# Kernel optimization log

Hardware: AMD Instinct MI355X
Metric: run time of the kernel (lower is better)

## Reference

```python
import jax, jax.numpy as jnp
import numpy as np

H = 16        # num attention heads
KVH = 4       # num key/value heads
D = 128       # head dim
WIN = 1024    # sliding window (in packed per-state positions)
THETA = 10000.0
NUM_STATES = 8


def rotate_half(x):
    half = x.shape[-1] // 2
    return jnp.concatenate([-x[..., half:], x[..., :half]], axis=-1)


def setup_inputs() -> dict:
    key = jax.random.key(0)
    ks = jax.random.split(key, 6)
    B, L, HID = 2, 2048, 2048
    s = 0.02
    hidden_states = jax.random.normal(ks[0], (B, L, HID), jnp.float32)
    Wq = jax.random.normal(ks[1], (H * D, HID), jnp.float32) * s
    Wk = jax.random.normal(ks[2], (KVH * D, HID), jnp.float32) * s
    Wv = jax.random.normal(ks[3], (KVH * D, HID), jnp.float32) * s
    Wo = jax.random.normal(ks[4], (HID, H * D), jnp.float32) * s
    sid = jax.random.randint(ks[5], (B, L), 0, NUM_STATES).astype(jnp.int64)
    position_ids = jnp.tile(jnp.arange(L, dtype=jnp.int64)[None, :], (B, 1))
    return dict(hidden_states=hidden_states, Wq=Wq, Wk=Wk, Wv=Wv, Wo=Wo,
                sid=sid, position_ids=position_ids)


def reference(hidden_states, Wq, Wk, Wv, Wo, sid, position_ids):
    B, L, HID = hidden_states.shape
    # projections (Linear without bias: x @ W.T)
    q = (hidden_states @ Wq.T).reshape(B, L, H, D)
    k = (hidden_states @ Wk.T).reshape(B, L, KVH, D)
    v = (hidden_states @ Wv.T).reshape(B, L, KVH, D)
    # rotary embedding
    inv_freq = 1.0 / (THETA ** (jnp.arange(0, D, 2, dtype=jnp.float32) / D))
    freqs = position_ids.astype(jnp.float32)[:, :, None] * inv_freq[None, None, :]  # [B,L,D/2]
    emb = jnp.concatenate([freqs, freqs], axis=-1)                                  # [B,L,D]
    cos = jnp.cos(emb)[:, :, None, :].astype(hidden_states.dtype)
    sin = jnp.sin(emb)[:, :, None, :].astype(hidden_states.dtype)
    q = q * cos + rotate_half(q) * sin
    k = k * cos + rotate_half(k) * sin
    # GQA: repeat kv heads (repeat_interleave along head dim)
    n_rep = H // KVH
    k = jnp.repeat(k, n_rep, axis=2)  # [B,L,H,D]
    v = jnp.repeat(v, n_rep, axis=2)
    # BoSs mask: attend within same state id, causal, sliding window over
    # packed-per-state rank distance (equivalent to the varlen packing path)
    same = sid[:, :, None] == sid[:, None, :]                  # [B,L,L]
    tril = jnp.tril(jnp.ones((L, L), dtype=bool))[None]        # [1,L,L]
    rank = jnp.sum(same & tril, axis=-1) - 1                   # [B,L] rank within own state
    win_ok = (rank[:, :, None] - rank[:, None, :]) <= WIN
    mask = same & tril & win_ok                                # [B,L,L]
    scale = D ** -0.5
    scores = jnp.einsum('bqhd,bkhd->bhqk', q, k) * scale       # [B,H,L,L]
    scores = jnp.where(mask[:, None, :, :], scores, jnp.finfo(scores.dtype).min)
    attn = jax.nn.softmax(scores, axis=-1)
    o = jnp.einsum('bhqk,bkhd->bqhd', attn, v).reshape(B, L, H * D)
    return o @ Wo.T
```

## Files before the change

### kernel.cpp

```cpp
#include <hip/hip_runtime.h>
#include <hip/hip_bf16.h>

#define H_ 16
#define KVH_ 4
#define D_ 128
#define L_ 2048
#define B_ 2
#define HID_ 2048
#define WIN_ 1024
#define NS_ 8
#define QKV_N 3072

typedef __attribute__((ext_vector_type(8))) short short8;
typedef __attribute__((ext_vector_type(4))) float floatx4;

__device__ inline float bf16_to_f(unsigned short u) {
    union { unsigned int i; float f; } c; c.i = ((unsigned int)u) << 16; return c.f;
}
__device__ inline unsigned short f_to_bf16(float f) {
    __hip_bfloat16 h = __float2bfloat16(f);
    return *(unsigned short*)&h;
}

__device__ inline int world_is_bf16(const unsigned short* hs_u) {
    int lane = threadIdx.x & 63;
    unsigned short u = hs_u[(lane & 31) * 2];
    int e = (u >> 7) & 0xFF;
    unsigned long long bad = __ballot(e > 130);
    return bad == 0ULL;
}
__device__ inline int pid_stride(const int* pids) { return (pids[1] == 0) ? 2 : 1; }

__global__ __launch_bounds__(256) void convert_all(const void* __restrict__ hs,
                                                   const void* __restrict__ Wq,
                                                   const void* __restrict__ Wk,
                                                   const void* __restrict__ Wv,
                                                   const void* __restrict__ Wo,
                                                   unsigned short* __restrict__ c_hs,
                                                   unsigned short* __restrict__ c_Wq,
                                                   unsigned short* __restrict__ c_Wk,
                                                   unsigned short* __restrict__ c_Wv,
                                                   unsigned short* __restrict__ c_Wo) {
    int isbf = world_is_bf16((const unsigned short*)hs);
    if (isbf) return;
    const int N0 = (B_ * L_ * HID_) / 4;
    const int N1 = (HID_ * HID_) / 4;
    const int N2 = (KVH_ * D_ * HID_) / 4;
    const int N3 = N2;
    const int N4 = N1;
    const int total = N0 + N1 + N2 + N3 + N4;
    for (int i = blockIdx.x * 256 + threadIdx.x; i < total; i += gridDim.x * 256) {
        int j = i;
        const void* src; unsigned short* dst;
        if (j < N0)              { src = hs; dst = c_hs; }
        else if ((j -= N0) < N1) { src = Wq; dst = c_Wq; }
        else if ((j -= N1) < N2) { src = Wk; dst = c_Wk; }
        else if ((j -= N2) < N3) { src = Wv; dst = c_Wv; }
        else                     { j -= N3; src = Wo; dst = c_Wo; }
        float4 f = ((const float4*)src)[j];
        ushort4 o4;
        o4.x = f_to_bf16(f.x); o4.y = f_to_bf16(f.y);
        o4.z = f_to_bf16(f.z); o4.w = f_to_bf16(f.w);
        ((ushort4*)dst)[j] = o4;
    }
}

__global__ __launch_bounds__(256) void scan_kernel(const int* __restrict__ sid,
                                                   const int* __restrict__ pids,
                                                   int* __restrict__ rank,
                                                   int* __restrict__ poslist,
                                                   int* __restrict__ counts) {
    int stride = pid_stride(pids);
    int b = blockIdx.x;
    int t = threadIdx.x;
    __shared__ int cnt[256][NS_];
    __shared__ int pre[256][NS_];
    const int* s = sid + (size_t)b * L_ * stride;
    int myid[8];
#pragma unroll
    for (int i = 0; i < 8; i++) myid[i] = s[(t * 8 + i) * stride];
#pragma unroll
    for (int st = 0; st < NS_; st++) cnt[t][st] = 0;
#pragma unroll
    for (int i = 0; i < 8; i++) cnt[t][myid[i]]++;
    __syncthreads();
    for (int off = 1; off < 256; off <<= 1) {
        int add[NS_];
        if (t >= off)
#pragma unroll
            for (int st = 0; st < NS_; st++) add[st] = cnt[t - off][st];
        __syncthreads();
        if (t >= off)
#pragma unroll
            for (int st = 0; st < NS_; st++) cnt[t][st] += add[st];
        __syncthreads();
    }
#pragma unroll
    for (int st = 0; st < NS_; st++) pre[t][st] = t ? cnt[t - 1][st] : 0;
    if (t == 255)
#pragma unroll
        for (int st = 0; st < NS_; st++) counts[b * NS_ + st] = cnt[255][st];
    __syncthreads();
#pragma unroll
    for (int i = 0; i < 8; i++) {
        int sd = myid[i];
        int r = pre[t][sd]++;
        int pos = t * 8 + i;
        rank[b * L_ + pos] = r;
        poslist[((size_t)b * NS_ + sd) * L_ + r] = pos;
    }
}

#define STAGE(gptr, ldsdst)                                                     \
    __builtin_amdgcn_global_load_lds(                                           \
        (const __attribute__((address_space(1))) unsigned int*)(gptr),          \
        (__attribute__((address_space(3))) unsigned int*)(ldsdst), 16, 0, 0)

#define SB __builtin_amdgcn_sched_barrier(0)

#define MFMA_P(P)                                                               \
    __builtin_amdgcn_s_setprio(1);                                              \
    _Pragma("unroll")                                                           \
    for (int m2 = 0; m2 < 2; ++m2)                                              \
        _Pragma("unroll")                                                       \
        for (int nt = 0; nt < 4; ++nt)                                          \
            acc[(P) * 2 + m2][nt] = __builtin_amdgcn_mfma_f32_16x16x32_bf16(    \
                fA[(P) * 2 + m2], fB[nt], acc[(P) * 2 + m2][nt], 0, 0, 0);      \
    __builtin_amdgcn_s_setprio(0)

template<int MT>
__global__ __launch_bounds__(512, 1) void gemm_t(const unsigned short* __restrict__ Ac,
                                                 const unsigned short* __restrict__ B0c,
                                                 const unsigned short* __restrict__ B1c,
                                                 const unsigned short* __restrict__ B2c,
                                                 const unsigned short* __restrict__ Aa,
                                                 const unsigned short* __restrict__ B0a,
                                                 const unsigned short* __restrict__ B1a,
                                                 const unsigned short* __restrict__ B2a,
                                                 void* __restrict__ C,
                                                 int M, int N, int K,
                                                 int nb1, int nb2,
                                                 const unsigned short* __restrict__ hs_probe,
                                                 int c_mode) {
    const int CH_A = MT / 2;
    __shared__ unsigned short As[4][MT * 2048];
    __shared__ unsigned short Bs[4][8192];
    int tid = threadIdx.x;
    int wave = tid >> 6, lane = tid & 63;
    int quad = lane >> 4, l16 = lane & 15;
    int wr = wave >> 2, wc = wave & 3;
    int bn_t = blockIdx.x;
    int bm = blockIdx.y * (MT * 64), bn = bn_t * 256;

    int isbf = world_is_bf16(hs_probe);
    const unsigned short* A  = isbf ? Aa  : Ac;
    const unsigned short* B0 = isbf ? B0a : B0c;
    const unsigned short* B1 = isbf ? B1a : B1c;
    const unsigned short* B2 = isbf ? B2a : B2c;

    const unsigned short* Bseg;
    int brow0;
    if (bn_t < nb1)      { Bseg = B0; brow0 = bn; }
    else if (bn_t < nb2) { Bseg = B1; brow0 = bn - nb1 * 256; }
    else                 { Bseg = B2; brow0 = bn - nb2 * 256; }

    int sub = tid >> 2, slot = tid & 3;
    int swz = slot ^ ((sub >> 1) & 3);
    unsigned int a_off[CH_A], b_off[2];
#pragma unroll
    for (int c = 0; c < CH_A; ++c)
        a_off[c] = (unsigned int)((bm + c * 128 + sub) * K + swz * 8);
#pragma unroll
    for (int c = 0; c < 2; ++c)
        b_off[c] = (unsigned int)((brow0 + c * 128 + sub) * K + swz * 8);

    const int arow = wr * (MT * 32) + l16;
    const int brr  = wc * 64 + l16;
    const int xr   = (l16 >> 1) & 3;

    floatx4 acc[2 * MT][4] = {};
    short8 fA[2 * MT], fB[4];
    const int KT = K >> 5;

#pragma unroll
    for (int pt = 0; pt < 3; ++pt) {
        unsigned int kel = (unsigned int)pt * 32;
#pragma unroll
        for (int c = 0; c < 2; ++c)
            STAGE(Bseg + b_off[c] + kel, &Bs[pt][c * 4096 + tid * 8]);
#pragma unroll
        for (int c = 0; c < CH_A; ++c)
            STAGE(A + a_off[c] + kel, &As[pt][c * 4096 + tid * 8]);
    }

    for (int t = 0; t < KT; ++t) {
        const unsigned short* Ab = As[t & 3];
        const unsigned short* Bb = Bs[t & 3];
        int nbuf = (t + 3) & 3;
        int t3 = (t + 3 < KT) ? t + 3 : KT - 1;
        unsigned int kel = (unsigned int)t3 * 32;

        if constexpr (MT == 4) asm volatile("s_waitcnt vmcnt(8)" ::: "memory");
        else                   asm volatile("s_waitcnt vmcnt(6)" ::: "memory");
        __builtin_amdgcn_s_barrier();
        asm volatile("" ::: "memory");

#pragma unroll
        for (int nt = 0; nt < 4; ++nt)
            fB[nt] = *(const short8*)&Bb[(brr + nt * 16) * 32 + ((quad ^ xr) * 8)];
#pragma unroll
        for (int mt = 0; mt < 2 * MT; ++mt)
            fA[mt] = *(const short8*)&Ab[(arow + mt * 16) * 32 + ((quad ^ xr) * 8)];
        SB;

#pragma unroll
        for (int c = 0; c < 2; ++c)
            STAGE(Bseg + b_off[c] + kel, &Bs[nbuf][c * 4096 + tid * 8]);
#pragma unroll
        for (int c = 0; c < CH_A; ++c)
            STAGE(A + a_off[c] + kel, &As[nbuf][c * 4096 + tid * 8]);
        SB;

        MFMA_P(0); SB;
        MFMA_P(1);
        if constexpr (MT == 4) {
            SB; MFMA_P(2); SB; MFMA_P(3);
        }
    }
    asm volatile("s_waitcnt vmcnt(0)" ::: "memory");

    int cf32 = c_mode ? !isbf : 0;
#pragma unroll
    for (int a = 0; a < 2 * MT; ++a)
#pragma unroll
        for (int g = 0; g < 4; ++g)
#pragma unroll
            for (int r = 0; r < 4; ++r) {
                int row = bm + wr * (MT * 32) + a * 16 + quad * 4 + r;
                int col = bn + wc * 64 + g * 16 + l16;
                size_t idx = (size_t)row * N + col;
                if (cf32) ((float*)C)[idx] = acc[a][g][r];
                else      ((unsigned short*)C)[idx] = f_to_bf16(acc[a][g][r]);
            }
}

__global__ __launch_bounds__(256) void rope_kernel(unsigned short* __restrict__ qkv,
                                                   const int* __restrict__ pos_ids) {
    int stride = pid_stride(pos_ids);
    int idx = blockIdx.x * 256 + threadIdx.x;
    int i = idx & 31;
    int tmp = idx >> 5;
    int head = tmp % 20;
    int bl = tmp / 20;
    if (bl >= B_ * L_) return;
    float posf = (float)pos_ids[bl * stride];
    const float k = (2.0f / 128.0f) * 13.287712379549449f;
    float inv0 = exp2f(-(float)(2 * i) * k);
    float inv1 = exp2f(-(float)(2 * i + 1) * k);
    float a0 = posf * inv0, a1 = posf * inv1;
    float c0 = cosf(a0), s0 = sinf(a0);
    float c1 = cosf(a1), s1 = sinf(a1);
    unsigned short* p = qkv + (size_t)bl * QKV_N +
                        ((head < H_) ? head * D_ : 2048 + (head - H_) * D_);
    ushort2 lo = *(const ushort2*)(p + 2 * i);
    ushort2 hi = *(const ushort2*)(p + 2 * i + 64);
    float x0a = bf16_to_f(lo.x), x0b = bf16_to_f(lo.y);
    float x1a = bf16_to_f(hi.x), x1b = bf16_to_f(hi.y);
    ushort2 olo, ohi;
    olo.x = f_to_bf16(x0a * c0 - x1a * s0);
    olo.y = f_to_bf16(x0b * c1 - x1b * s1);
    ohi.x = f_to_bf16(x1a * c0 + x0a * s0);
    ohi.y = f_to_bf16(x1b * c1 + x0b * s1);
    *(ushort2*)(p + 2 * i)      = olo;
    *(ushort2*)(p + 2 * i + 64) = ohi;
}

__global__ __launch_bounds__(256, 4) void attn_mfma(const unsigned short* __restrict__ qkv,
                                                    const int* __restrict__ counts,
                                                    const int* __restrict__ poslist,
                                                    unsigned short* __restrict__ o) {
    int qt  = blockIdx.x & 127;
    int kvh = (blockIdx.x >> 7) & 3;
    int s   = (blockIdx.x >> 9) & 7;
    int b   = blockIdx.x >> 12;
    int n = counts[b * NS_ + s];
    if (qt * 16 >= n) return;
    const int* plist = poslist + ((size_t)b * NS_ + s) * L_;

    __shared__ short Ksh[32][136];
    __shared__ short Vsh[128][40];
    __shared__ short Psh[4][16][40];
    __shared__ int posq[16];

    int tid = threadIdx.x;
    int wave = tid >> 6, lane = tid & 63;
    int quad = lane >> 4, l16 = lane & 15;
    int h = kvh * 4 + wave;
    const float scale = 0.08838834764831845f;

    if (tid < 16) posq[tid] = plist[min(qt * 16 + tid, n - 1)];
    __syncthreads();

    short8 qf[4];
    {
        const unsigned short* gq =
            qkv + ((size_t)(b << 11) + posq[l16]) * QKV_N + h * D_;
#pragma unroll
        for (int kk = 0; kk < 4; kk++)
            qf[kk] = *(const short8*)(gq + kk * 32 + quad * 8);
    }

    float m_r[4], l_r[4];
    floatx4 Ov[8];
#pragma unroll
    for (int r4 = 0; r4 < 4; r4++) { m_r[r4] = -1e30f; l_r[r4] = 0.f; }
#pragma unroll
    for (int nt = 0; nt < 8; nt++) Ov[nt] = (floatx4){0.f, 0.f, 0.f, 0.f};

    int c0 = max(0, (qt * 16 - WIN_) >> 5);
    int nch = ((qt * 16 + 15) >> 5) + 1;

    int r = tid >> 3, seg = tid & 7;
    int vc = r ^ ((seg & 3) << 3);
    short8 kr0, kr1, vr0, vr1;
    {
        int kpos = plist[min(c0 * 32 + r, n - 1)];
        size_t base = ((size_t)(b << 11) + kpos) * QKV_N + 2048 + kvh * D_ + seg * 16;
        kr0 = *(const short8*)(qkv + base);
        kr1 = *(const short8*)(qkv + base + 8);
        vr0 = *(const short8*)(qkv + base + 512);
        vr1 = *(const short8*)(qkv + base + 520);
    }

    for (int c = c0; c < nch; c++) {
        *(short8*)&Ksh[r][seg * 16]     = kr0;
        *(short8*)&Ksh[r][seg * 16 + 8] = kr1;
#pragma unroll
        for (int e = 0; e < 8; e++) Vsh[seg * 16 + e][vc] = vr0[e];
#pragma unroll
        for (int e = 0; e < 8; e++) Vsh[seg * 16 + 8 + e][vc] = vr1[e];
        __syncthreads();

        if (c + 1 < nch) {
            int kpos = plist[min((c + 1) * 32 + r, n - 1)];
            size_t base = ((size_t)(b << 11) + kpos) * QKV_N + 2048 + kvh * D_ + seg * 16;
            kr0 = *(const short8*)(qkv + base);
            kr1 = *(const short8*)(qkv + base + 8);
            vr0 = *(const short8*)(qkv + base + 512);
            vr1 = *(const short8*)(qkv + base + 520);
        }

        floatx4 s0 = (floatx4){0.f, 0.f, 0.f, 0.f};
        floatx4 s1 = (floatx4){0.f, 0.f, 0.f, 0.f};
#pragma unroll
        for (int kk = 0; kk < 4; kk++) {
            short8 kfa = *(const short8*)&Ksh[l16][kk * 32 + quad * 8];
            s0 = __builtin_amdgcn_mfma_f32_16x16x32_bf16(qf[kk], kfa, s0, 0, 0, 0);
        }
#pragma unroll
        for (int kk = 0; kk < 4; kk++) {
            short8 kfb = *(const short8*)&Ksh[16 + l16][kk * 32 + quad * 8];
            s1 = __builtin_amdgcn_mfma_f32_16x16x32_bf16(qf[kk], kfb, s1, 0, 0, 0);
        }

        int kr0i = c * 32 + l16, kr1i = kr0i + 16;
        float x0[4], x1[4], rmax[4];
#pragma unroll
        for (int r4 = 0; r4 < 4; r4++) {
            int qr = qt * 16 + quad * 4 + r4;
            bool mk0 = (kr0i <= qr) && (kr0i >= qr - WIN_);
            bool mk1 = (kr1i <= qr) && (kr1i >= qr - WIN_);
            x0[r4] = mk0 ? s0[r4] * scale : -1e30f;
            x1[r4] = mk1 ? s1[r4] * scale : -1e30f;
            rmax[r4] = fmaxf(x0[r4], x1[r4]);
        }
#pragma unroll
        for (int st = 1; st <= 8; st <<= 1)
#pragma unroll
            for (int r4 = 0; r4 < 4; r4++)
                rmax[r4] = fmaxf(rmax[r4], __shfl_xor(rmax[r4], st, 64));
        float al[4], psum[4];
#pragma unroll
        for (int r4 = 0; r4 < 4; r4++) {
            float nm = fmaxf(m_r[r4], rmax[r4]);
            al[r4] = __expf(m_r[r4] - nm);
            m_r[r4] = nm;
            x0[r4] = (x0[r4] > -1e29f) ? __expf(x0[r4] - nm) : 0.f;
            x1[r4] = (x1[r4] > -1e29f) ? __expf(x1[r4] - nm) : 0.f;
            psum[r4] = x0[r4] + x1[r4];
        }
#pragma unroll
        for (int st = 1; st <= 8; st <<= 1)
#pragma unroll
            for (int r4 = 0; r4 < 4; r4++)
                psum[r4] += __shfl_xor(psum[r4], st, 64);
#pragma unroll
        for (int r4 = 0; r4 < 4; r4++) l_r[r4] = l_r[r4] * al[r4] + psum[r4];
#pragma unroll
        for (int nt = 0; nt < 8; nt++)
#pragma unroll
            for (int r4 = 0; r4 < 4; r4++) Ov[nt][r4] *= al[r4];

#pragma unroll
        for (int r4 = 0; r4 < 4; r4++) {
            Psh[wave][quad * 4 + r4][l16]      = (short)f_to_bf16(x0[r4]);
            Psh[wave][quad * 4 + r4][16 + l16] = (short)f_to_bf16(x1[r4]);
        }
        short8 pf = *(const short8*)&Psh[wave][l16][quad * 8];

#pragma unroll
        for (int nt = 0; nt < 8; nt++) {
            short8 vf = *(const short8*)&Vsh[nt * 16 + l16][(quad ^ (nt & 3)) * 8];
            Ov[nt] = __builtin_amdgcn_mfma_f32_16x16x32_bf16(pf, vf, Ov[nt], 0, 0, 0);
        }
        __syncthreads();
    }

    float inv_r[4];
    int pos_r[4], qvalid[4];
#pragma unroll
    for (int r4 = 0; r4 < 4; r4++) {
        int qr = qt * 16 + quad * 4 + r4;
        qvalid[r4] = (qr < n);
        inv_r[r4] = 1.f / l_r[r4];
        pos_r[r4] = posq[quad * 4 + r4];
    }
#pragma unroll
    for (int nt = 0; nt < 8; nt++)
#pragma unroll
        for (int r4 = 0; r4 < 4; r4++)
            if (qvalid[r4])
                o[(((size_t)(b << 11) + pos_r[r4]) * H_ + h) * D_ + nt * 16 + l16] =
                    f_to_bf16(Ov[nt][r4] * inv_r[r4]);
}

extern "C" void kernel_launch(void* const* d_in, const int* in_sizes, int n_in,
                              void* d_out, int out_size, void* d_ws, size_t ws_size,
                              hipStream_t stream) {
    const void* hs = d_in[0];
    const void* Wq = d_in[1];
    const void* Wk = d_in[2];
    const void* Wv = d_in[3];
    const void* Wo = d_in[4];
    const int* sid  = (const int*)d_in[5];
    const int* pids = (const int*)d_in[6];

    const int M = B_ * L_;
    char* w = (char*)d_ws;
    unsigned short* qkv  = (unsigned short*)(w + 256);
    unsigned short* o_b  = (unsigned short*)(w + 25166080);
    unsigned short* c_hs = (unsigned short*)(w + 41943296);
    unsigned short* c_Wq = (unsigned short*)(w + 58720512);
    unsigned short* c_Wk = (unsigned short*)(w + 67109120);
    unsigned short* c_Wv = (unsigned short*)(w + 69206272);
    unsigned short* c_Wo = (unsigned short*)(w + 71303424);
    int* rank            = (int*)(w + 79692032);
    int* plist           = (int*)(w + 79708416);
    int* counts          = (int*)(w + 79839488);

    const unsigned short* hs_probe = (const unsigned short*)hs;

    convert_all<<<2048, 256, 0, stream>>>(hs, Wq, Wk, Wv, Wo,
                                          c_hs, c_Wq, c_Wk, c_Wv, c_Wo);

    scan_kernel<<<B_, 256, 0, stream>>>(sid, pids, rank, plist, counts);

    gemm_t<4><<<dim3(QKV_N / 256, M / 256), 512, 0, stream>>>(
        c_hs, c_Wq, c_Wk, c_Wv,
        (const unsigned short*)hs, (const unsigned short*)Wq,
        (const unsigned short*)Wk, (const unsigned short*)Wv,
        qkv, M, QKV_N, HID_, 8, 10, hs_probe, 0);

    int rope_threads = M * (H_ + KVH_) * 32;
    rope_kernel<<<(rope_threads + 255) / 256, 256, 0, stream>>>(qkv, pids);

    attn_mfma<<<B_ * NS_ * KVH_ * (L_ / 16), 256, 0, stream>>>(qkv, counts, plist, o_b);

    gemm_t<2><<<dim3(HID_ / 256, M / 128), 512, 0, stream>>>(
        o_b, c_Wo, c_Wo, c_Wo,
        o_b, (const unsigned short*)Wo, (const unsigned short*)Wo,
        (const unsigned short*)Wo,
        d_out, M, HID_, HID_, 1 << 30, 1 << 30, hs_probe, 1);
}
```

Before: 293.5 us.

## Fuse rotary embedding into QKV GEMM epilogue via permuted B rows

Removes the separate rope kernel and applies rotary embedding in the QKV GEMM epilogue. B tile rows are permuted at load time so each lane holds paired dimensions d and d+64 in its accumulators, letting it rotate in registers before the bf16 store. This saves one full read and write pass over the QKV buffer plus a kernel launch. In exchange the epilogue gains per-row position loads and sin/cos work, and the stores become strided.

```diff
diff --git a/kernel.cpp b/kernel.cpp
--- a/kernel.cpp
+++ b/kernel.cpp
@@ -128,7 +128,7 @@
                 fA[(P) * 2 + m2], fB[nt], acc[(P) * 2 + m2][nt], 0, 0, 0);      \
     __builtin_amdgcn_s_setprio(0)
 
-template<int MT>
+template<int MT, bool ROPE>
 __global__ __launch_bounds__(512, 1) void gemm_t(const unsigned short* __restrict__ Ac,
                                                  const unsigned short* __restrict__ B0c,
                                                  const unsigned short* __restrict__ B1c,
@@ -141,7 +141,8 @@
                                                  int M, int N, int K,
                                                  int nb1, int nb2,
                                                  const unsigned short* __restrict__ hs_probe,
-                                                 int c_mode) {
+                                                 int c_mode,
+                                                 const int* __restrict__ pids) {
     const int CH_A = MT / 2;
     __shared__ unsigned short As[4][MT * 2048];
     __shared__ unsigned short Bs[4][8192];
@@ -166,13 +167,18 @@
 
     int sub = tid >> 2, slot = tid & 3;
     int swz = slot ^ ((sub >> 1) & 3);
+    int tsub = sub;
+    if constexpr (ROPE) {
+        int wdd = sub >> 6, gg = (sub >> 4) & 3, ll = sub & 15;
+        tsub = (gg & 1) * 16 + ll + wdd * 32 + (gg >> 1) * 64;
+    }
     unsigned int a_off[CH_A], b_off[2];
 #pragma unroll
     for (int c = 0; c < CH_A; ++c)
         a_off[c] = (unsigned int)((bm + c * 128 + sub) * K + swz * 8);
 #pragma unroll
     for (int c = 0; c < 2; ++c)
-        b_off[c] = (unsigned int)((brow0 + c * 128 + sub) * K + swz * 8);
+        b_off[c] = (unsigned int)((brow0 + c * 128 + tsub) * K + swz * 8);
 
     const int arow = wr * (MT * 32) + l16;
     const int brr  = wc * 64 + l16;
@@ -229,50 +235,53 @@
     }
     asm volatile("s_waitcnt vmcnt(0)" ::: "memory");
 
-    int cf32 = c_mode ? !isbf : 0;
-#pragma unroll
-    for (int a = 0; a < 2 * MT; ++a)
-#pragma unroll
-        for (int g = 0; g < 4; ++g)
+    if constexpr (ROPE) {
+        int strideP = pid_stride(pids);
+        int hb = (bn >> 7) + (wc >> 1);
+        bool qk = (hb < 20);
+        int w = wc & 1;
+        int d0 = l16 + w * 32;
+        const float kc = 0.015625f * 13.287712379549449f;
+        float inv0 = exp2f(-(float)d0 * kc);
+        float inv1 = exp2f(-(float)(d0 + 16) * kc);
+        int colbase = bn + (wc >> 1) * 128 + w * 32 + l16;
+#pragma unroll
+        for (int a = 0; a < 2 * MT; ++a)
 #pragma unroll
             for (int r = 0; r < 4; ++r) {
                 int row = bm + wr * (MT * 32) + a * 16 + quad * 4 + r;
-                int col = bn + wc * 64 + g * 16 + l16;
-                size_t idx = (size_t)row * N + col;
-                if (cf32) ((float*)C)[idx] = acc[a][g][r];
-                else      ((unsigned short*)C)[idx] = f_to_bf16(acc[a][g][r]);
+                float x0 = acc[a][0][r], x1 = acc[a][1][r];
+                float x2 = acc[a][2][r], x3 = acc[a][3][r];
+                if (qk) {
+                    float pos = (float)pids[row * strideP];
+                    float a0 = pos * inv0, a1 = pos * inv1;
+                    float c0 = cosf(a0), s0 = sinf(a0);
+                    float c1 = cosf(a1), s1 = sinf(a1);
+                    float n0 = x0 * c0 - x2 * s0, n2 = x2 * c0 + x0 * s0;
+                    float n1 = x1 * c1 - x3 * s1, n3 = x3 * c1 + x1 * s1;
+                    x0 = n0; x1 = n1; x2 = n2; x3 = n3;
+                }
+                unsigned short* Cp = (unsigned short*)C + (size_t)row * N + colbase;
+                Cp[0]  = f_to_bf16(x0);
+                Cp[16] = f_to_bf16(x1);
+                Cp[64] = f_to_bf16(x2);
+                Cp[80] = f_to_bf16(x3);
             }
-}
-
-__global__ __launch_bounds__(256) void rope_kernel(unsigned short* __restrict__ qkv,
-                                                   const int* __restrict__ pos_ids) {
-    int stride = pid_stride(pos_ids);
-    int idx = blockIdx.x * 256 + threadIdx.x;
-    int i = idx & 31;
-    int tmp = idx >> 5;
-    int head = tmp % 20;
-    int bl = tmp / 20;
-    if (bl >= B_ * L_) return;
-    float posf = (float)pos_ids[bl * stride];
-    const float k = (2.0f / 128.0f) * 13.287712379549449f;
-    float inv0 = exp2f(-(float)(2 * i) * k);
-    float inv1 = exp2f(-(float)(2 * i + 1) * k);
-    float a0 = posf * inv0, a1 = posf * inv1;
-    float c0 = cosf(a0), s0 = sinf(a0);
-    float c1 = cosf(a1), s1 = sinf(a1);
-    unsigned short* p = qkv + (size_t)bl * QKV_N +
-                        ((head < H_) ? head * D_ : 2048 + (head - H_) * D_);
-    ushort2 lo = *(const ushort2*)(p + 2 * i);
-    ushort2 hi = *(const ushort2*)(p + 2 * i + 64);
-    float x0a = bf16_to_f(lo.x), x0b = bf16_to_f(lo.y);
-    float x1a = bf16_to_f(hi.x), x1b = bf16_to_f(hi.y);
-    ushort2 olo, ohi;
-    olo.x = f_to_bf16(x0a * c0 - x1a * s0);
-    olo.y = f_to_bf16(x0b * c1 - x1b * s1);
-    ohi.x = f_to_bf16(x1a * c0 + x0a * s0);
-    ohi.y = f_to_bf16(x1b * c1 + x0b * s1);
-    *(ushort2*)(p + 2 * i)      = olo;
-    *(ushort2*)(p + 2 * i + 64) = ohi;
+    } else {
+        int cf32 = c_mode ? !isbf : 0;
+#pragma unroll
+        for (int a = 0; a < 2 * MT; ++a)
+#pragma unroll
+            for (int g = 0; g < 4; ++g)
+#pragma unroll
+                for (int r = 0; r < 4; ++r) {
+                    int row = bm + wr * (MT * 32) + a * 16 + quad * 4 + r;
+                    int col = bn + wc * 64 + g * 16 + l16;
+                    size_t idx = (size_t)row * N + col;
+                    if (cf32) ((float*)C)[idx] = acc[a][g][r];
+                    else      ((unsigned short*)C)[idx] = f_to_bf16(acc[a][g][r]);
+                }
+    }
 }
 
 __global__ __launch_bounds__(256, 4) void attn_mfma(const unsigned short* __restrict__ qkv,
@@ -465,20 +474,17 @@
 
     scan_kernel<<<B_, 256, 0, stream>>>(sid, pids, rank, plist, counts);
 
-    gemm_t<4><<<dim3(QKV_N / 256, M / 256), 512, 0, stream>>>(
+    gemm_t<4, true><<<dim3(QKV_N / 256, M / 256), 512, 0, stream>>>(
         c_hs, c_Wq, c_Wk, c_Wv,
         (const unsigned short*)hs, (const unsigned short*)Wq,
         (const unsigned short*)Wk, (const unsigned short*)Wv,
-        qkv, M, QKV_N, HID_, 8, 10, hs_probe, 0);
-
-    int rope_threads = M * (H_ + KVH_) * 32;
-    rope_kernel<<<(rope_threads + 255) / 256, 256, 0, stream>>>(qkv, pids);
+        qkv, M, QKV_N, HID_, 8, 10, hs_probe, 0, pids);
 
     attn_mfma<<<B_ * NS_ * KVH_ * (L_ / 16), 256, 0, stream>>>(qkv, counts, plist, o_b);
 
-    gemm_t<2><<<dim3(HID_ / 256, M / 128), 512, 0, stream>>>(
+    gemm_t<2, false><<<dim3(HID_ / 256, M / 128), 512, 0, stream>>>(
         o_b, c_Wo, c_Wo, c_Wo,
         o_b, (const unsigned short*)Wo, (const unsigned short*)Wo,
         (const unsigned short*)Wo,
-        d_out, M, HID_, HID_, 1 << 30, 1 << 30, hs_probe, 1);
-}
+        d_out, M, HID_, HID_, 1 << 30, 1 << 30, hs_probe, 1, pids);
+}
```

Measured after the change: 316.2 us. +7.8%, slower.
